# Kernel tuning notes

Measured on AMD Instinct MI355X. Metric: run time of the kernel, lower is better.

The kernel has to match this reference:

```python
import jax, jax.numpy as jnp
import numpy as np

N_NODES = 50000
N_EDGES = 600000
N_GRAPHS = 64
N_LAYERS = 4
D = 128
BN_EPS = 1e-5


def setup_inputs() -> dict:
    key = jax.random.key(0)
    ks = jax.random.split(key, 12)
    inp = {
        'x_node': jax.random.randint(ks[0], (N_NODES, 1), 0, 119, dtype=jnp.int64) if jax.config.jax_enable_x64 else jax.random.randint(ks[0], (N_NODES, 1), 0, 119).astype(jnp.int32),
        'edge_index': jax.random.randint(ks[1], (2, N_EDGES), 0, N_NODES).astype(jnp.int32),
        'batch': jnp.sort(jax.random.randint(ks[2], (N_NODES,), 0, N_GRAPHS)).astype(jnp.int32),
        'emb_table': jax.random.normal(ks[3], (119, D), jnp.float32),
        'conv_w1': jax.random.normal(ks[4], (N_LAYERS, D, D), jnp.float32) * 0.05,
        'conv_b1': jnp.zeros((N_LAYERS, D), jnp.float32),
        'bn1_g': jnp.ones((N_LAYERS, D), jnp.float32),
        'bn1_b': jnp.zeros((N_LAYERS, D), jnp.float32),
        'conv_w2': jax.random.normal(ks[5], (N_LAYERS, D, D), jnp.float32) * 0.05,
        'conv_b2': jnp.zeros((N_LAYERS, D), jnp.float32),
        'bn2_g': jnp.ones((N_LAYERS, D), jnp.float32),
        'bn2_b': jnp.zeros((N_LAYERS, D), jnp.float32),
        'lin1_w': jax.random.normal(ks[6], (D, 2 * D), jnp.float32) * 0.05,
        'lin1_b': jnp.zeros((2 * D,), jnp.float32),
        'lin2_w': jax.random.normal(ks[7], (2 * D, 10), jnp.float32) * 0.05,
        'lin2_b': jnp.zeros((10,), jnp.float32),
    }
    return inp


def _bn(h, g, b):
    # BatchNorm1d over the node axis (training-mode batch statistics, biased var)
    mu = jnp.mean(h, axis=0, keepdims=True)
    var = jnp.mean((h - mu) ** 2, axis=0, keepdims=True)
    return (h - mu) * jax.lax.rsqrt(var + BN_EPS) * g + b


def reference(x_node, edge_index, batch, emb_table, conv_w1, conv_b1, bn1_g, bn1_b,
              conv_w2, conv_b2, bn2_g, bn2_b, lin1_w, lin1_b, lin2_w, lin2_b):
    x = emb_table[x_node[:, 0]]                      # [N, D] node embedding
    src, dst = edge_index[0], edge_index[1]          # j, i in the torch code
    eps = 0.0
    for l in range(N_LAYERS):
        msg = x[src]                                 # gather x_j, [E, D]
        agg = jax.ops.segment_sum(msg, dst, num_segments=N_NODES)  # scatter-add to targets
        h = agg + (1.0 + eps) * x
        h = jax.nn.relu(_bn(h @ conv_w1[l] + conv_b1[l], bn1_g[l], bn1_b[l]))
        h = jax.nn.relu(_bn(h @ conv_w2[l] + conv_b2[l], bn2_g[l], bn2_b[l]))
        x = h
    # jump_mode=None -> last layer; readout: per-graph mean pooling
    ones = jnp.ones((N_NODES,), x.dtype)
    counts = jax.ops.segment_sum(ones, batch, num_segments=N_GRAPHS)
    pooled = jax.ops.segment_sum(x, batch, num_segments=N_GRAPHS)
    pooled = pooled / jnp.maximum(counts, 1.0)[:, None]             # [B, D]
    out = jax.nn.relu(pooled @ lin1_w + lin1_b)
    return out @ lin2_w + lin2_b                     # [B, 10]
```

## Files before the change

### kernel.cpp

```cpp
#include <hip/hip_runtime.h>
#include <hip/hip_fp16.h>

#define N_NODES 50000
#define N_EDGES 600000
#define N_GRAPHS 64
#define N_LAYERS 4
#define D 128
#define BN_EPS 1e-5f

#define SCAN_NB 49
#define GB 782

typedef __attribute__((ext_vector_type(8))) short short8;
typedef __attribute__((ext_vector_type(8))) _Float16 half8;
typedef __attribute__((ext_vector_type(4))) float f32x4;

#define WLO_SCALE 2048.0f
#define WLO_INV (1.0f / 2048.0f)

__device__ __forceinline__ float half_bits_to_f32(short b) {
  union { unsigned short u; __half h; } cv;
  cv.u = (unsigned short)b;
  return __half2float(cv.h);
}
__device__ __forceinline__ unsigned short f32_to_half_bits(float f) {
  union { __half h; unsigned short u; } cv;
  cv.h = __float2half(f);
  return cv.u;
}

__global__ __launch_bounds__(256) void embed_kernel(const int* __restrict__ idx,
    const float* __restrict__ emb, __half* __restrict__ xh) {
  int tid = blockIdx.x * 256 + threadIdx.x;
  if (tid >= N_NODES * 32) return;
  int n = tid >> 5, c4 = tid & 31;
  int e = idx[n];
  float4 v = ((const float4*)emb)[(size_t)e * 32 + c4];
  __half2 a = __float22half2_rn(make_float2(v.x, v.y));
  __half2 b = __float22half2_rn(make_float2(v.z, v.w));
  ((__half2*)xh)[(size_t)tid * 2] = a;
  ((__half2*)xh)[(size_t)tid * 2 + 1] = b;
}

__global__ __launch_bounds__(256) void count_kernel(const int* __restrict__ dst,
    int* __restrict__ counts) {
  int e = blockIdx.x * 256 + threadIdx.x;
  if (e < N_EDGES) atomicAdd(&counts[dst[e]], 1);
}

__global__ __launch_bounds__(256) void scan_block_kernel(const int* __restrict__ counts,
    int* __restrict__ offsets, int* __restrict__ partials) {
  __shared__ int s[256];
  int t = threadIdx.x;
  int base = blockIdx.x * 1024 + t * 4;
  int v[4];
#pragma unroll
  for (int i = 0; i < 4; ++i) v[i] = (base + i < N_NODES) ? counts[base + i] : 0;
  int tsum = v[0] + v[1] + v[2] + v[3];
  s[t] = tsum;
  __syncthreads();
  for (int off = 1; off < 256; off <<= 1) {
    int add = (t >= off) ? s[t - off] : 0;
    __syncthreads();
    s[t] += add;
    __syncthreads();
  }
  int run = s[t] - tsum;
#pragma unroll
  for (int i = 0; i < 4; ++i) {
    if (base + i < N_NODES) offsets[base + i] = run;
    run += v[i];
  }
  if (t == 255) partials[blockIdx.x] = s[255];
}

__global__ void scan_partials_kernel(int* partials) {
  if (threadIdx.x == 0) {
    int run = 0;
    for (int b = 0; b < SCAN_NB; ++b) { int v = partials[b]; partials[b] = run; run += v; }
  }
}

__global__ __launch_bounds__(256) void add_offsets_kernel(int* __restrict__ offsets,
    const int* __restrict__ partials, int* __restrict__ cursor) {
  int i = blockIdx.x * 256 + threadIdx.x;
  if (i < N_NODES) {
    int o = offsets[i] + partials[i >> 10];
    offsets[i] = o;
    cursor[i] = o;
  }
  if (blockIdx.x == 0 && threadIdx.x == 0) offsets[N_NODES] = N_EDGES;
}

__global__ __launch_bounds__(256) void fill_csr_kernel(const int* __restrict__ src,
    const int* __restrict__ dst, int* __restrict__ cursor, int* __restrict__ col) {
  int e = blockIdx.x * 256 + threadIdx.x;
  if (e < N_EDGES) {
    int d = dst[e];
    int p = atomicAdd(&cursor[d], 1);
    col[p] = src[e];
  }
}

template <bool TRANS>
__global__ __launch_bounds__(256) void agg_kernel(const __half* __restrict__ xh,
    const int* __restrict__ offsets, const int* __restrict__ col,
    const float* __restrict__ scale, const float* __restrict__ shift,
    __half* __restrict__ h) {
  int node = blockIdx.x * 4 + (threadIdx.x >> 6);
  int lane = threadIdx.x & 63;
  float2 scl, shl;
  if (TRANS) {
    scl = ((const float2*)scale)[lane];
    shl = ((const float2*)shift)[lane];
  }
  const __half2* x2 = (const __half2*)xh;
  float2 self = __half22float2(x2[(size_t)node * 64 + lane]);
  float2 acc;
  if (TRANS) {
    acc.x = fmaxf(fmaf(self.x, scl.x, shl.x), 0.f);
    acc.y = fmaxf(fmaf(self.y, scl.y, shl.y), 0.f);
  } else {
    acc = self;
  }
  int beg = offsets[node], end = offsets[node + 1];
  for (int e = beg; e < end; e += 8) {
    int idx[8];
    bool val[8];
#pragma unroll
    for (int j = 0; j < 8; ++j) {
      val[j] = (e + j) < end;
      idx[j] = val[j] ? (e + j) : e;
    }
    int sidx[8];
#pragma unroll
    for (int j = 0; j < 8; ++j) sidx[j] = col[idx[j]];
    float2 ff[8];
#pragma unroll
    for (int j = 0; j < 8; ++j) ff[j] = __half22float2(x2[(size_t)sidx[j] * 64 + lane]);
#pragma unroll
    for (int j = 0; j < 8; ++j) {
      float2 v = ff[j];
      if (TRANS) {
        v.x = fmaxf(fmaf(v.x, scl.x, shl.x), 0.f);
        v.y = fmaxf(fmaf(v.y, scl.y, shl.y), 0.f);
      }
      if (val[j]) {
        acc.x += v.x;
        acc.y += v.y;
      }
    }
  }
  ((__half2*)h)[(size_t)node * 64 + lane] = __float22half2_rn(acc);
}

__global__ __launch_bounds__(256) void repack_w_kernel(const float* __restrict__ cw1,
    const float* __restrict__ cw2, unsigned short* __restrict__ Wh,
    unsigned short* __restrict__ Wl) {
  int b = blockIdx.x;
  int l = b >> 1, which = b & 1;
  const float* Wm = (which ? cw2 : cw1) + (size_t)l * D * D;
  unsigned short* outh = Wh + (size_t)b * D * D;
  unsigned short* outl = Wl + (size_t)b * D * D;
  for (int T = threadIdx.x; T < 2048; T += 256) {
    int ks = T >> 9, ct = (T >> 6) & 7, lane = T & 63;
    int kbase = ks * 32 + ((lane >> 4) << 3);
    int c = ct * 16 + (lane & 15);
    unsigned short hs[8], ls[8];
#pragma unroll
    for (int e = 0; e < 8; ++e) {
      float v = Wm[(size_t)(kbase + e) * D + c];
      __half hh = __float2half_rn(v);
      float rem = v - __half2float(hh);
      __half hl = __float2half_rn(rem * WLO_SCALE);
      union { __half h; unsigned short u; } c1, c2;
      c1.h = hh; c2.h = hl;
      hs[e] = c1.u;
      ls[e] = c2.u;
    }
    *(ushort4*)(outh + (size_t)T * 8)     = *(ushort4*)&hs[0];
    *(ushort4*)(outh + (size_t)T * 8 + 4) = *(ushort4*)&hs[4];
    *(ushort4*)(outl + (size_t)T * 8)     = *(ushort4*)&ls[0];
    *(ushort4*)(outl + (size_t)T * 8 + 4) = *(ushort4*)&ls[4];
  }
}

template <bool TRANS>
__global__ __launch_bounds__(256) void gemm_f16_kernel(
    const __half* __restrict__ A, const unsigned short* __restrict__ Wh,
    const unsigned short* __restrict__ Wl, const float* __restrict__ bias,
    const float* __restrict__ scale, const float* __restrict__ shift,
    __half* __restrict__ Y, float* __restrict__ ps, float* __restrict__ pq) {
  __shared__ unsigned short AL[64][136];
  int t = threadIdx.x;
  int row0 = blockIdx.x * 64;
  int lane = t & 63;
  int wv = t >> 6;

#pragma unroll
  for (int i = 0; i < 4; ++i) {
    int s = i * 256 + t;
    int r = s >> 4, c8 = s & 15;
    int row = row0 + r;
    short8 v = {0, 0, 0, 0, 0, 0, 0, 0};
    if (row < N_NODES) v = *(const short8*)(A + (size_t)row * D + c8 * 8);
    if (TRANS) {
      float4 sc0 = ((const float4*)scale)[c8 * 2];
      float4 sc1 = ((const float4*)scale)[c8 * 2 + 1];
      float4 sh0 = ((const float4*)shift)[c8 * 2];
      float4 sh1 = ((const float4*)shift)[c8 * 2 + 1];
      float scv[8] = {sc0.x, sc0.y, sc0.z, sc0.w, sc1.x, sc1.y, sc1.z, sc1.w};
      float shv[8] = {sh0.x, sh0.y, sh0.z, sh0.w, sh1.x, sh1.y, sh1.z, sh1.w};
      short8 o;
#pragma unroll
      for (int j = 0; j < 8; ++j) {
        float f = fmaxf(fmaf(half_bits_to_f32(v[j]), scv[j], shv[j]), 0.f);
        o[j] = (short)f32_to_half_bits(f);
      }
      v = o;
    }
    *(short8*)&AL[r][c8 * 8] = v;
  }
  __syncthreads();

  f32x4 acch[4][2], accl[4][2];
#pragma unroll
  for (int rt = 0; rt < 4; ++rt)
#pragma unroll
    for (int c = 0; c < 2; ++c) {
      acch[rt][c] = (f32x4){0.f, 0.f, 0.f, 0.f};
      accl[rt][c] = (f32x4){0.f, 0.f, 0.f, 0.f};
    }

  int arow_lo = lane & 15;
  int kgrp = (lane >> 4) * 8;
#pragma unroll
  for (int ks = 0; ks < 4; ++ks) {
    size_t wbase = ((size_t)(ks * 8 + wv * 2) * 64 + lane) * 8;
    half8 wh0 = __builtin_bit_cast(half8, *(const short8*)(Wh + wbase));
    half8 wl0 = __builtin_bit_cast(half8, *(const short8*)(Wl + wbase));
    half8 wh1 = __builtin_bit_cast(half8, *(const short8*)(Wh + wbase + 512));
    half8 wl1 = __builtin_bit_cast(half8, *(const short8*)(Wl + wbase + 512));
#pragma unroll
    for (int rt = 0; rt < 4; ++rt) {
      half8 av = __builtin_bit_cast(half8,
          *(const short8*)&AL[rt * 16 + arow_lo][ks * 32 + kgrp]);
      acch[rt][0] = __builtin_amdgcn_mfma_f32_16x16x32_f16(av, wh0, acch[rt][0], 0, 0, 0);
      accl[rt][0] = __builtin_amdgcn_mfma_f32_16x16x32_f16(av, wl0, accl[rt][0], 0, 0, 0);
      acch[rt][1] = __builtin_amdgcn_mfma_f32_16x16x32_f16(av, wh1, acch[rt][1], 0, 0, 0);
      accl[rt][1] = __builtin_amdgcn_mfma_f32_16x16x32_f16(av, wl1, accl[rt][1], 0, 0, 0);
    }
  }

  __syncthreads();

  int rsub = (lane >> 4) << 2;
  int cl = lane & 15;
#pragma unroll
  for (int cti = 0; cti < 2; ++cti) {
    int c = wv * 32 + cti * 16 + cl;
    float b = bias[c];
    float s = 0.f, q = 0.f;
#pragma unroll
    for (int rt = 0; rt < 4; ++rt) {
#pragma unroll
      for (int r = 0; r < 4; ++r) {
        int rl = rt * 16 + rsub + r;
        float y = fmaf(accl[rt][cti][r], WLO_INV, acch[rt][cti][r]) + b;
        ((__half*)&AL[rl][0])[c] = __float2half(y);
        if (row0 + rl < N_NODES) {
          s += y;
          q += y * y;
        }
      }
    }
    s += __shfl_xor(s, 16, 64);
    s += __shfl_xor(s, 32, 64);
    q += __shfl_xor(q, 16, 64);
    q += __shfl_xor(q, 32, 64);
    if (lane < 16) {
      ps[(size_t)blockIdx.x * 128 + c] = s;
      pq[(size_t)blockIdx.x * 128 + c] = q;
    }
  }
  __syncthreads();
#pragma unroll
  for (int i = 0; i < 4; ++i) {
    int s = i * 256 + t;
    int r = s >> 4, c8 = s & 15;
    int row = row0 + r;
    if (row < N_NODES) {
      ushort4 a = *(ushort4*)&AL[r][c8 * 8];
      ushort4 b = *(ushort4*)&AL[r][c8 * 8 + 4];
      *(ushort4*)((unsigned short*)Y + (size_t)row * D + c8 * 8)     = a;
      *(ushort4*)((unsigned short*)Y + (size_t)row * D + c8 * 8 + 4) = b;
    }
  }
}

__global__ __launch_bounds__(256) void finalize_kernel(const float* __restrict__ ps,
    const float* __restrict__ pq, const float* __restrict__ g, const float* __restrict__ b,
    float* __restrict__ scale, float* __restrict__ shift) {
  int c = blockIdx.x;
  int t = threadIdx.x;
  float s = 0.f, q = 0.f;
  for (int i = t; i < GB; i += 256) {
    s += ps[(size_t)i * 128 + c];
    q += pq[(size_t)i * 128 + c];
  }
#pragma unroll
  for (int o = 1; o < 64; o <<= 1) {
    s += __shfl_xor(s, o, 64);
    q += __shfl_xor(q, o, 64);
  }
  __shared__ float rs[4], rq[4];
  if ((t & 63) == 0) { rs[t >> 6] = s; rq[t >> 6] = q; }
  __syncthreads();
  if (t == 0) {
    s = rs[0] + rs[1] + rs[2] + rs[3];
    q = rq[0] + rq[1] + rq[2] + rq[3];
    float mu = s * (1.0f / N_NODES);
    float var = fmaxf(q * (1.0f / N_NODES) - mu * mu, 0.f);
    float sc = g[c] * rsqrtf(var + BN_EPS);
    scale[c] = sc;
    shift[c] = fmaf(-mu, sc, b[c]);
  }
}

__device__ __forceinline__ int lower_bound_batch(const int* __restrict__ batch, int key) {
  int lo = 0, hi = N_NODES;
  while (lo < hi) {
    int mid = (lo + hi) >> 1;
    if (batch[mid] < key) lo = mid + 1; else hi = mid;
  }
  return lo;
}

__global__ __launch_bounds__(256) void pool_kernel(const __half* __restrict__ x,
    const int* __restrict__ batch, const float* __restrict__ scale,
    const float* __restrict__ shift, float* __restrict__ pp, float* __restrict__ gcnt) {
  int g = blockIdx.x, chunk = blockIdx.y;
  int lo = lower_bound_batch(batch, g);
  int hi = lower_bound_batch(batch, g + 1);
  int f = threadIdx.x & 127, sub = threadIdx.x >> 7;
  float sc = scale[f], sh = shift[f];
  int cnt = hi - lo;
  int per = (cnt + 7) >> 3;
  int s = lo + chunk * per;
  int e = min(s + per, hi);
  float acc = 0.f;
  for (int n = s + sub; n < e; n += 2)
    acc += fmaxf(fmaf(__half2float(x[(size_t)n * 128 + f]), sc, sh), 0.f);
  __shared__ float red[2][128];
  red[sub][f] = acc;
  __syncthreads();
  if (sub == 0) pp[((size_t)g * 8 + chunk) * 128 + f] = red[0][f] + red[1][f];
  if (threadIdx.x == 0 && chunk == 0) gcnt[g] = (float)cnt;
}

__global__ __launch_bounds__(256) void mlp_kernel(const float* __restrict__ pp,
    const float* __restrict__ gcnt, const float* __restrict__ w1, const float* __restrict__ b1,
    const float* __restrict__ w2, const float* __restrict__ b2, float* __restrict__ out) {
  int g = blockIdx.x, t = threadIdx.x;
  __shared__ float p[128];
  __shared__ float hbuf[256];
  if (t < 128) {
    float s = 0.f;
#pragma unroll
    for (int c = 0; c < 8; ++c) s += pp[((size_t)g * 8 + c) * 128 + t];
    p[t] = s / fmaxf(gcnt[g], 1.0f);
  }
  __syncthreads();
  float acc = b1[t];
  for (int k = 0; k < 128; ++k) acc = fmaf(p[k], w1[k * 256 + t], acc);
  hbuf[t] = fmaxf(acc, 0.f);
  __syncthreads();
  if (t < 10) {
    float o = b2[t];
    for (int k = 0; k < 256; ++k) o = fmaf(hbuf[k], w2[k * 10 + t], o);
    out[g * 10 + t] = o;
  }
}

extern "C" void kernel_launch(void* const* d_in, const int* in_sizes, int n_in,
                              void* d_out, int out_size, void* d_ws, size_t ws_size,
                              hipStream_t stream) {
  const int* x_node = (const int*)d_in[0];
  const int* eidx = (const int*)d_in[1];
  const int* batch = (const int*)d_in[2];
  const float* emb = (const float*)d_in[3];
  const float* cw1 = (const float*)d_in[4];
  const float* cb1 = (const float*)d_in[5];
  const float* bn1g = (const float*)d_in[6];
  const float* bn1b = (const float*)d_in[7];
  const float* cw2 = (const float*)d_in[8];
  const float* cb2 = (const float*)d_in[9];
  const float* bn2g = (const float*)d_in[10];
  const float* bn2b = (const float*)d_in[11];
  const float* l1w = (const float*)d_in[12];
  const float* l1b = (const float*)d_in[13];
  const float* l2w = (const float*)d_in[14];
  const float* l2b = (const float*)d_in[15];
  float* out = (float*)d_out;

  char* ws = (char*)d_ws;
  size_t off = 0;
  auto carve = [&](size_t bytes) -> void* {
    void* p = ws + off;
    off += (bytes + 255) & ~(size_t)255;
    return p;
  };
  __half* xh   = (__half*)carve((size_t)N_NODES * D * 2);
  __half* abuf = (__half*)carve((size_t)N_NODES * D * 2);
  __half* ybuf = (__half*)carve((size_t)N_NODES * D * 2);
  __half* zbuf = (__half*)carve((size_t)N_NODES * D * 2);
  int* counts = (int*)carve((size_t)N_NODES * 4);
  int* offsets = (int*)carve((size_t)(N_NODES + 1) * 4);
  int* cursor = (int*)carve((size_t)N_NODES * 4);
  int* col = (int*)carve((size_t)N_EDGES * 4);
  int* partials = (int*)carve(64 * 4);
  float* part_s = (float*)carve((size_t)GB * 128 * 4);
  float* part_q = (float*)carve((size_t)GB * 128 * 4);
  float* scaleb = (float*)carve(8 * 128 * 4);
  float* shiftb = (float*)carve(8 * 128 * 4);
  float* pp = (float*)carve(64 * 8 * 128 * 4);
  float* gcnt = (float*)carve(64 * 4);
  unsigned short* Whb = (unsigned short*)carve((size_t)8 * D * D * 2);
  unsigned short* Wlb = (unsigned short*)carve((size_t)8 * D * D * 2);
  (void)ws_size;
  (void)in_sizes;
  (void)n_in;
  (void)out_size;

  const int* srcp = eidx;
  const int* dstp = eidx + N_EDGES;

  hipMemsetAsync(counts, 0, (size_t)N_NODES * 4, stream);

  repack_w_kernel<<<8, 256, 0, stream>>>(cw1, cw2, Whb, Wlb);
  embed_kernel<<<6250, 256, 0, stream>>>(x_node, emb, xh);
  count_kernel<<<(N_EDGES + 255) / 256, 256, 0, stream>>>(dstp, counts);
  scan_block_kernel<<<SCAN_NB, 256, 0, stream>>>(counts, offsets, partials);
  scan_partials_kernel<<<1, 64, 0, stream>>>(partials);
  add_offsets_kernel<<<(N_NODES + 255) / 256, 256, 0, stream>>>(offsets, partials, cursor);
  fill_csr_kernel<<<(N_EDGES + 255) / 256, 256, 0, stream>>>(srcp, dstp, cursor, col);

  for (int l = 0; l < N_LAYERS; ++l) {
    float* sc1 = scaleb + (l * 2) * 128;
    float* sh1 = shiftb + (l * 2) * 128;
    float* sc2 = scaleb + (l * 2 + 1) * 128;
    float* sh2 = shiftb + (l * 2 + 1) * 128;
    const float* scp = scaleb + (l * 2 - 1) * 128;
    const float* shp = shiftb + (l * 2 - 1) * 128;
    const unsigned short* W1h = Whb + (size_t)(l * 2) * D * D;
    const unsigned short* W1l = Wlb + (size_t)(l * 2) * D * D;
    const unsigned short* W2h = Whb + (size_t)(l * 2 + 1) * D * D;
    const unsigned short* W2l = Wlb + (size_t)(l * 2 + 1) * D * D;

    if (l == 0)
      agg_kernel<false><<<12500, 256, 0, stream>>>(xh, offsets, col, nullptr, nullptr, abuf);
    else
      agg_kernel<true><<<12500, 256, 0, stream>>>(zbuf, offsets, col, scp, shp, abuf);
    gemm_f16_kernel<false><<<GB, 256, 0, stream>>>(abuf, W1h, W1l, cb1 + l * D,
                                                   nullptr, nullptr, ybuf, part_s, part_q);
    finalize_kernel<<<128, 256, 0, stream>>>(part_s, part_q, bn1g + l * D, bn1b + l * D,
                                             sc1, sh1);
    gemm_f16_kernel<true><<<GB, 256, 0, stream>>>(ybuf, W2h, W2l, cb2 + l * D,
                                                  sc1, sh1, zbuf, part_s, part_q);
    finalize_kernel<<<128, 256, 0, stream>>>(part_s, part_q, bn2g + l * D, bn2b + l * D,
                                             sc2, sh2);
  }

  pool_kernel<<<dim3(64, 8), 256, 0, stream>>>(zbuf, batch,
      scaleb + 7 * 128, shiftb + 7 * 128, pp, gcnt);
  mlp_kernel<<<64, 256, 0, stream>>>(pp, gcnt, l1w, l1b, l2w, l2b, out);
}
```

Baseline: 355.4 us.

## Fuse BN finalize into GEMM via atomic buckets and last-block ticket; merge setup kernels

The separate BN finalize kernels are removed. Each GEMM block now atomically adds its per-column sums into 32 buckets, and the last block to arrive, detected with a ticket counter, computes scale and shift and then resets the buckets. Embedding, memset, and weight repacking are merged into one setup kernel, and the partials scan is folded into add_offsets. Together this drops about ten kernel launches, at the cost of float atomics (nondeterministic summation order) and a threadfence/ticket serialization at the end of each GEMM.

```diff
diff --git a/kernel.cpp b/kernel.cpp
--- a/kernel.cpp
+++ b/kernel.cpp
@@ -10,6 +10,11 @@
 
 #define SCAN_NB 49
 #define GB 782
+#define NBUCKET 32
+
+#define EMB_NB 6250
+#define ZERO_NB 14
+#define RPK_NB 8
 
 typedef __attribute__((ext_vector_type(8))) short short8;
 typedef __attribute__((ext_vector_type(8))) _Float16 half8;
@@ -29,17 +34,60 @@
   return cv.u;
 }
 
-__global__ __launch_bounds__(256) void embed_kernel(const int* __restrict__ idx,
-    const float* __restrict__ emb, __half* __restrict__ xh) {
-  int tid = blockIdx.x * 256 + threadIdx.x;
-  if (tid >= N_NODES * 32) return;
-  int n = tid >> 5, c4 = tid & 31;
-  int e = idx[n];
-  float4 v = ((const float4*)emb)[(size_t)e * 32 + c4];
-  __half2 a = __float22half2_rn(make_float2(v.x, v.y));
-  __half2 b = __float22half2_rn(make_float2(v.z, v.w));
-  ((__half2*)xh)[(size_t)tid * 2] = a;
-  ((__half2*)xh)[(size_t)tid * 2 + 1] = b;
+__global__ __launch_bounds__(256) void setup_kernel(const int* __restrict__ idx,
+    const float* __restrict__ emb, __half* __restrict__ xh,
+    int* __restrict__ counts, float* __restrict__ bsum, float* __restrict__ bsq,
+    int* __restrict__ ticket, const float* __restrict__ cw1,
+    const float* __restrict__ cw2, unsigned short* __restrict__ Wh,
+    unsigned short* __restrict__ Wl) {
+  int bb = blockIdx.x;
+  int t = threadIdx.x;
+  if (bb < EMB_NB) {
+    int tid = bb * 256 + t;
+    if (tid >= N_NODES * 32) return;
+    int n = tid >> 5, c4 = tid & 31;
+    int e = idx[n];
+    float4 v = ((const float4*)emb)[(size_t)e * 32 + c4];
+    __half2 a = __float22half2_rn(make_float2(v.x, v.y));
+    __half2 b = __float22half2_rn(make_float2(v.z, v.w));
+    ((__half2*)xh)[(size_t)tid * 2] = a;
+    ((__half2*)xh)[(size_t)tid * 2 + 1] = b;
+  } else if (bb < EMB_NB + ZERO_NB) {
+    int tid = (bb - EMB_NB) * 256 + t;
+    for (int i = tid; i < N_NODES; i += ZERO_NB * 256) counts[i] = 0;
+    for (int i = tid; i < NBUCKET * 128; i += ZERO_NB * 256) {
+      bsum[i] = 0.f;
+      bsq[i] = 0.f;
+    }
+    if (tid == 0) *ticket = 0;
+  } else {
+    int b = bb - (EMB_NB + ZERO_NB);
+    int l = b >> 1, which = b & 1;
+    const float* Wm = (which ? cw2 : cw1) + (size_t)l * D * D;
+    unsigned short* outh = Wh + (size_t)b * D * D;
+    unsigned short* outl = Wl + (size_t)b * D * D;
+    for (int T = t; T < 2048; T += 256) {
+      int ks = T >> 9, ct = (T >> 6) & 7, lane = T & 63;
+      int kbase = ks * 32 + ((lane >> 4) << 3);
+      int c = ct * 16 + (lane & 15);
+      unsigned short hs[8], ls[8];
+#pragma unroll
+      for (int e = 0; e < 8; ++e) {
+        float v = Wm[(size_t)(kbase + e) * D + c];
+        __half hh = __float2half_rn(v);
+        float rem = v - __half2float(hh);
+        __half hl = __float2half_rn(rem * WLO_SCALE);
+        union { __half h; unsigned short u; } c1, c2;
+        c1.h = hh; c2.h = hl;
+        hs[e] = c1.u;
+        ls[e] = c2.u;
+      }
+      *(ushort4*)(outh + (size_t)T * 8)     = *(ushort4*)&hs[0];
+      *(ushort4*)(outh + (size_t)T * 8 + 4) = *(ushort4*)&hs[4];
+      *(ushort4*)(outl + (size_t)T * 8)     = *(ushort4*)&ls[0];
+      *(ushort4*)(outl + (size_t)T * 8 + 4) = *(ushort4*)&ls[4];
+    }
+  }
 }
 
 __global__ __launch_bounds__(256) void count_kernel(const int* __restrict__ dst,
@@ -74,22 +122,25 @@
   if (t == 255) partials[blockIdx.x] = s[255];
 }
 
-__global__ void scan_partials_kernel(int* partials) {
-  if (threadIdx.x == 0) {
-    int run = 0;
-    for (int b = 0; b < SCAN_NB; ++b) { int v = partials[b]; partials[b] = run; run += v; }
-  }
-}
-
 __global__ __launch_bounds__(256) void add_offsets_kernel(int* __restrict__ offsets,
     const int* __restrict__ partials, int* __restrict__ cursor) {
-  int i = blockIdx.x * 256 + threadIdx.x;
+  __shared__ int pre[SCAN_NB];
+  int t = threadIdx.x;
+  if (t < SCAN_NB) pre[t] = partials[t];
+  __syncthreads();
+  if (t == 0) {
+    int run = 0;
+#pragma unroll
+    for (int b = 0; b < SCAN_NB; ++b) { int v = pre[b]; pre[b] = run; run += v; }
+  }
+  __syncthreads();
+  int i = blockIdx.x * 256 + t;
   if (i < N_NODES) {
-    int o = offsets[i] + partials[i >> 10];
+    int o = offsets[i] + pre[i >> 10];
     offsets[i] = o;
     cursor[i] = o;
   }
-  if (blockIdx.x == 0 && threadIdx.x == 0) offsets[N_NODES] = N_EDGES;
+  if (blockIdx.x == 0 && t == 0) offsets[N_NODES] = N_EDGES;
 }
 
 __global__ __launch_bounds__(256) void fill_csr_kernel(const int* __restrict__ src,
@@ -154,43 +205,15 @@
   ((__half2*)h)[(size_t)node * 64 + lane] = __float22half2_rn(acc);
 }
 
-__global__ __launch_bounds__(256) void repack_w_kernel(const float* __restrict__ cw1,
-    const float* __restrict__ cw2, unsigned short* __restrict__ Wh,
-    unsigned short* __restrict__ Wl) {
-  int b = blockIdx.x;
-  int l = b >> 1, which = b & 1;
-  const float* Wm = (which ? cw2 : cw1) + (size_t)l * D * D;
-  unsigned short* outh = Wh + (size_t)b * D * D;
-  unsigned short* outl = Wl + (size_t)b * D * D;
-  for (int T = threadIdx.x; T < 2048; T += 256) {
-    int ks = T >> 9, ct = (T >> 6) & 7, lane = T & 63;
-    int kbase = ks * 32 + ((lane >> 4) << 3);
-    int c = ct * 16 + (lane & 15);
-    unsigned short hs[8], ls[8];
-#pragma unroll
-    for (int e = 0; e < 8; ++e) {
-      float v = Wm[(size_t)(kbase + e) * D + c];
-      __half hh = __float2half_rn(v);
-      float rem = v - __half2float(hh);
-      __half hl = __float2half_rn(rem * WLO_SCALE);
-      union { __half h; unsigned short u; } c1, c2;
-      c1.h = hh; c2.h = hl;
-      hs[e] = c1.u;
-      ls[e] = c2.u;
-    }
-    *(ushort4*)(outh + (size_t)T * 8)     = *(ushort4*)&hs[0];
-    *(ushort4*)(outh + (size_t)T * 8 + 4) = *(ushort4*)&hs[4];
-    *(ushort4*)(outl + (size_t)T * 8)     = *(ushort4*)&ls[0];
-    *(ushort4*)(outl + (size_t)T * 8 + 4) = *(ushort4*)&ls[4];
-  }
-}
-
 template <bool TRANS>
 __global__ __launch_bounds__(256) void gemm_f16_kernel(
     const __half* __restrict__ A, const unsigned short* __restrict__ Wh,
     const unsigned short* __restrict__ Wl, const float* __restrict__ bias,
     const float* __restrict__ scale, const float* __restrict__ shift,
-    __half* __restrict__ Y, float* __restrict__ ps, float* __restrict__ pq) {
+    __half* __restrict__ Y, float* __restrict__ bsum, float* __restrict__ bsq,
+    int* __restrict__ ticket, const float* __restrict__ bng,
+    const float* __restrict__ bnb, float* __restrict__ oscale,
+    float* __restrict__ oshift) {
   __shared__ unsigned short AL[64][136];
   int t = threadIdx.x;
   int row0 = blockIdx.x * 64;
@@ -256,6 +279,7 @@
 
   int rsub = (lane >> 4) << 2;
   int cl = lane & 15;
+  int bucket = (blockIdx.x & (NBUCKET - 1)) * 128;
 #pragma unroll
   for (int cti = 0; cti < 2; ++cti) {
     int c = wv * 32 + cti * 16 + cl;
@@ -279,8 +303,8 @@
     q += __shfl_xor(q, 16, 64);
     q += __shfl_xor(q, 32, 64);
     if (lane < 16) {
-      ps[(size_t)blockIdx.x * 128 + c] = s;
-      pq[(size_t)blockIdx.x * 128 + c] = q;
+      atomicAdd(&bsum[bucket + c], s);
+      atomicAdd(&bsq[bucket + c], q);
     }
   }
   __syncthreads();
@@ -296,34 +320,32 @@
       *(ushort4*)((unsigned short*)Y + (size_t)row * D + c8 * 8 + 4) = b;
     }
   }
-}
-
-__global__ __launch_bounds__(256) void finalize_kernel(const float* __restrict__ ps,
-    const float* __restrict__ pq, const float* __restrict__ g, const float* __restrict__ b,
-    float* __restrict__ scale, float* __restrict__ shift) {
-  int c = blockIdx.x;
-  int t = threadIdx.x;
-  float s = 0.f, q = 0.f;
-  for (int i = t; i < GB; i += 256) {
-    s += ps[(size_t)i * 128 + c];
-    q += pq[(size_t)i * 128 + c];
-  }
-#pragma unroll
-  for (int o = 1; o < 64; o <<= 1) {
-    s += __shfl_xor(s, o, 64);
-    q += __shfl_xor(q, o, 64);
-  }
-  __shared__ float rs[4], rq[4];
-  if ((t & 63) == 0) { rs[t >> 6] = s; rq[t >> 6] = q; }
-  __syncthreads();
-  if (t == 0) {
-    s = rs[0] + rs[1] + rs[2] + rs[3];
-    q = rq[0] + rq[1] + rq[2] + rq[3];
-    float mu = s * (1.0f / N_NODES);
-    float var = fmaxf(q * (1.0f / N_NODES) - mu * mu, 0.f);
-    float sc = g[c] * rsqrtf(var + BN_EPS);
-    scale[c] = sc;
-    shift[c] = fmaf(-mu, sc, b[c]);
+
+  __threadfence();
+  __syncthreads();
+  __shared__ int islast;
+  if (t == 0) islast = (atomicAdd(ticket, 1) == GB - 1) ? 1 : 0;
+  __syncthreads();
+  if (islast) {
+    if (t < 128) {
+      float s = 0.f, q = 0.f;
+#pragma unroll
+      for (int i = 0; i < NBUCKET; ++i) {
+        s += bsum[i * 128 + t];
+        q += bsq[i * 128 + t];
+      }
+      float mu = s * (1.0f / N_NODES);
+      float var = fmaxf(q * (1.0f / N_NODES) - mu * mu, 0.f);
+      float sc = bng[t] * rsqrtf(var + BN_EPS);
+      oscale[t] = sc;
+      oshift[t] = fmaf(-mu, sc, bnb[t]);
+    }
+    __syncthreads();
+    for (int i = t; i < NBUCKET * 128; i += 256) {
+      bsum[i] = 0.f;
+      bsq[i] = 0.f;
+    }
+    if (t == 0) *ticket = 0;
   }
 }
 
@@ -419,8 +441,9 @@
   int* cursor = (int*)carve((size_t)N_NODES * 4);
   int* col = (int*)carve((size_t)N_EDGES * 4);
   int* partials = (int*)carve(64 * 4);
-  float* part_s = (float*)carve((size_t)GB * 128 * 4);
-  float* part_q = (float*)carve((size_t)GB * 128 * 4);
+  float* bsum = (float*)carve((size_t)NBUCKET * 128 * 4);
+  float* bsq = (float*)carve((size_t)NBUCKET * 128 * 4);
+  int* ticket = (int*)carve(256);
   float* scaleb = (float*)carve(8 * 128 * 4);
   float* shiftb = (float*)carve(8 * 128 * 4);
   float* pp = (float*)carve(64 * 8 * 128 * 4);
@@ -435,13 +458,10 @@
   const int* srcp = eidx;
   const int* dstp = eidx + N_EDGES;
 
-  hipMemsetAsync(counts, 0, (size_t)N_NODES * 4, stream);
-
-  repack_w_kernel<<<8, 256, 0, stream>>>(cw1, cw2, Whb, Wlb);
-  embed_kernel<<<6250, 256, 0, stream>>>(x_node, emb, xh);
+  setup_kernel<<<EMB_NB + ZERO_NB + RPK_NB, 256, 0, stream>>>(
+      x_node, emb, xh, counts, bsum, bsq, ticket, cw1, cw2, Whb, Wlb);
   count_kernel<<<(N_EDGES + 255) / 256, 256, 0, stream>>>(dstp, counts);
   scan_block_kernel<<<SCAN_NB, 256, 0, stream>>>(counts, offsets, partials);
-  scan_partials_kernel<<<1, 64, 0, stream>>>(partials);
   add_offsets_kernel<<<(N_NODES + 255) / 256, 256, 0, stream>>>(offsets, partials, cursor);
   fill_csr_kernel<<<(N_EDGES + 255) / 256, 256, 0, stream>>>(srcp, dstp, cursor, col);
 
@@ -462,13 +482,9 @@
     else
       agg_kernel<true><<<12500, 256, 0, stream>>>(zbuf, offsets, col, scp, shp, abuf);
     gemm_f16_kernel<false><<<GB, 256, 0, stream>>>(abuf, W1h, W1l, cb1 + l * D,
-                                                   nullptr, nullptr, ybuf, part_s, part_q);
-    finalize_kernel<<<128, 256, 0, stream>>>(part_s, part_q, bn1g + l * D, bn1b + l * D,
-                                             sc1, sh1);
+        nullptr, nullptr, ybuf, bsum, bsq, ticket, bn1g + l * D, bn1b + l * D, sc1, sh1);
     gemm_f16_kernel<true><<<GB, 256, 0, stream>>>(ybuf, W2h, W2l, cb2 + l * D,
-                                                  sc1, sh1, zbuf, part_s, part_q);
-    finalize_kernel<<<128, 256, 0, stream>>>(part_s, part_q, bn2g + l * D, bn2b + l * D,
-                                             sc2, sh2);
+        sc1, sh1, zbuf, bsum, bsq, ticket, bn2g + l * D, bn2b + l * D, sc2, sh2);
   }
 
   pool_kernel<<<dim3(64, 8), 256, 0, stream>>>(zbuf, batch,
```

Measured after the change: 991.5 us. 2.79x slower.
